# Kernel tuning notes

Measured on AMD Instinct MI355X. Metric: run time of the kernel, lower is better.

Reference implementation:

```python
import jax, jax.numpy as jnp
import numpy as np
from jax.scipy.special import digamma

N, D, K = 32768, 64, 64


def setup_inputs() -> dict:
    key = jax.random.key(0)
    k1, k2, k3, k4, k5, k6, k7 = jax.random.split(key, 7)
    X = jax.random.normal(k1, (N, D), dtype=jnp.float32)
    means = jax.random.normal(k2, (K, D), dtype=jnp.float32)
    # Upper-triangular precision Cholesky factors with strictly positive diagonal
    # (matches solve_triangular(L, I).T from the torch code).
    off = jnp.triu(jax.random.normal(k3, (K, D, D), dtype=jnp.float32) * 0.05, 1)
    diag = jnp.exp(jax.random.normal(k4, (K, D), dtype=jnp.float32) * 0.1)
    precisions_chol = off + jax.vmap(jnp.diag)(diag)
    weight_concentration = jax.random.uniform(k5, (2, K), dtype=jnp.float32, minval=0.5, maxval=5.0)
    # degrees_of_freedom must be > D - 1 so digamma args stay positive
    degrees_of_freedom = jnp.float32(D) + jax.random.uniform(k6, (K,), dtype=jnp.float32, minval=1.0, maxval=50.0)
    mean_precision = jax.random.uniform(k7, (K,), dtype=jnp.float32, minval=0.5, maxval=10.0)
    return {"X": X, "means": means, "precisions_chol": precisions_chol,
            "weight_concentration": weight_concentration,
            "degrees_of_freedom": degrees_of_freedom, "mean_precision": mean_precision}


def _weighted_log_prob(X, means, precisions_chol, weight_concentration,
                       degrees_of_freedom, mean_precision):
    n_features = X.shape[1]
    # log|prec_chol_k| = sum of log of diagonal entries
    log_det = jnp.sum(jnp.log(jnp.diagonal(precisions_chol, axis1=1, axis2=2)), axis=1)  # [K]
    # whitened residuals: y[n,k,:] = X[n] @ P_k - mu_k @ P_k
    XP = jnp.einsum('nd,kde->nke', X, precisions_chol)            # [N,K,D]
    muP = jnp.einsum('kd,kde->ke', means, precisions_chol)        # [K,D]
    sq = jnp.sum(jnp.square(XP - muP[None]), axis=-1)             # [N,K]
    log2pi = jnp.log(jnp.float32(2.0 * np.pi))
    log_gauss = -0.5 * (n_features * log2pi + sq) + log_det[None]
    # Bayesian corrections
    log_gauss = log_gauss - 0.5 * n_features * jnp.log(degrees_of_freedom)[None]
    i = jnp.arange(n_features, dtype=jnp.float32)
    log_lambda = n_features * jnp.log(jnp.float32(2.0)) + jnp.sum(
        digamma(0.5 * (degrees_of_freedom[None, :] - i[:, None])), axis=0)  # [K]
    log_prob = log_gauss + 0.5 * (log_lambda - n_features / mean_precision)[None]
    # stick-breaking log weights (dirichlet_process)
    a, b = weight_concentration[0], weight_concentration[1]
    dsum = digamma(a + b)
    log_w = digamma(a) - dsum + jnp.concatenate(
        [jnp.zeros((1,), dtype=X.dtype), jnp.cumsum(digamma(b) - dsum)[:-1]])
    return log_prob + log_w[None]


def reference(X, means, precisions_chol, weight_concentration,
              degrees_of_freedom, mean_precision):
    wlp = _weighted_log_prob(X, means, precisions_chol, weight_concentration,
                             degrees_of_freedom, mean_precision)
    return jnp.argmax(wlp, axis=1)
```

## Files before the change

### kernel.cpp

```cpp
#include <hip/hip_runtime.h>
#include <math.h>

#define N_ROWS 32768
#define DIM 64
#define KCOMP 64
#define KSPLIT 8
#define KLOCAL 8
#define THREADS 256
#define ROWS_PER_BLOCK 128
#define ROWS_PER_WAVE 32
#define ROWGROUPS (N_ROWS / ROWS_PER_BLOCK)

#define PT_K_BYTES 16384

#define LOG2PI_D 1.8378770664093454836

typedef _Float16 f16x8 __attribute__((ext_vector_type(8)));
typedef float f32x4 __attribute__((ext_vector_type(4)));

__device__ __forceinline__ double digamma_d(double x) {
  double r = 0.0;
  while (x < 6.0) { r -= 1.0 / x; x += 1.0; }
  double inv = 1.0 / x;
  double inv2 = inv * inv;
  double s = log(x) - 0.5 * inv
      - inv2 * (1.0/12.0 - inv2 * (1.0/120.0 - inv2 * (1.0/252.0
      - inv2 * (1.0/240.0 - inv2 * (1.0/132.0)))));
  return r + s;
}

__global__ void prep1_kernel(const float* __restrict__ means,
                             const float* __restrict__ P,
                             const float* __restrict__ wc,
                             const float* __restrict__ dof,
                             const float* __restrict__ mp,
                             char*   __restrict__ Pt,
                             float*  __restrict__ muP,
                             double* __restrict__ t_arr,
                             double* __restrict__ g_arr,
                             double* __restrict__ pc_arr)
{
  __shared__ float lds[DIM][DIM + 1];
  const int k = blockIdx.x;
  const int t = threadIdx.x;
  const float* Pk = P + k * DIM * DIM;

  for (int i = t; i < DIM * DIM; i += THREADS)
    lds[i >> 6][i & 63] = Pk[i];
  __syncthreads();

  char* dst = Pt + (size_t)k * PT_K_BYTES;
#pragma unroll
  for (int cc = 0; cc < 4; ++cc) {
    int cid  = cc * THREADS + t;
    int blk  = cid >> 7;
    int sel  = (cid >> 6) & 1;
    int lane = cid & 63;
    int et = blk >> 1, c = blk & 1;
    int m = lane & 15, q = lane >> 4;
    int e = et * 16 + m;
    int d0 = c * 32 + q * 8;
    f16x8 o;
#pragma unroll
    for (int j = 0; j < 8; ++j) {
      float v = lds[d0 + j][e];
      _Float16 h = (_Float16)v;
      o[j] = sel ? (_Float16)(v - (float)h) : h;
    }
    *(f16x8*)(dst + cid * 16) = o;
  }

  if (t < 64) {
    const int i = t;
    const float* mk = means + k * DIM;
    float acc = 0.f;
#pragma unroll 8
    for (int d = 0; d < DIM; ++d) acc = fmaf(mk[d], lds[d][i], acc);
    muP[k * DIM + i] = acc;

    double dofk = (double)dof[k];
    double s1 = digamma_d(0.5 * (dofk - (double)i));
    double s2 = log((double)lds[i][i]);
#pragma unroll
    for (int off = 32; off > 0; off >>= 1) {
      s1 += __shfl_down(s1, off);
      s2 += __shfl_down(s2, off);
    }
    if (i == 0) {
      double ak = (double)wc[k], bk = (double)wc[KCOMP + k];
      double dgab = digamma_d(ak + bk);
      double log_lambda = (double)DIM * log(2.0) + s1;
      double pc = s2
                - 0.5 * (double)DIM * LOG2PI_D
                - 0.5 * (double)DIM * log(dofk)
                + 0.5 * (log_lambda - (double)DIM / (double)mp[k]);
      t_arr[k] = digamma_d(bk) - dgab;
      g_arr[k] = digamma_d(ak) - dgab;
      pc_arr[k] = pc;
    }
  }
}

__global__ __launch_bounds__(THREADS, 4) void main_kernel(
    const float* __restrict__ X,
    const char*  __restrict__ Pt,
    const float* __restrict__ muP,
    const double* __restrict__ t_arr,
    const double* __restrict__ g_arr,
    const double* __restrict__ pc_arr,
    unsigned long long* __restrict__ packed,
    int* __restrict__ cnt,
    int* __restrict__ out)
{
  __shared__ float cvec_lds[KCOMP];
  __shared__ float mup_lds[KLOCAL * DIM];
  __shared__ int is_last;

  const int tid  = threadIdx.x;
  const int wave = tid >> 6;
  const int lane = tid & 63;
  const int m    = lane & 15;
  const int q    = lane >> 4;
  const int ks   = blockIdx.y;
  const int rowbase = blockIdx.x * ROWS_PER_BLOCK + wave * ROWS_PER_WAVE;

  if (tid < 64) {
    double t = t_arr[tid];
    double s = t;
#pragma unroll
    for (int off = 1; off < 64; off <<= 1) {
      double v = __shfl_up(s, off);
      if (tid >= off) s += v;
    }
    cvec_lds[tid] = (float)(pc_arr[tid] + g_arr[tid] + (s - t));
  }
  for (int i = tid; i < KLOCAL * DIM; i += THREADS)
    mup_lds[i] = muP[ks * KLOCAL * DIM + i];

  f16x8 ahi[2][2], alo[2][2];
#pragma unroll
  for (int rt = 0; rt < 2; ++rt) {
    int row = rowbase + rt * 16 + m;
    const float* xp = X + row * DIM;
#pragma unroll
    for (int c = 0; c < 2; ++c) {
      const float4* xq4 = (const float4*)(xp + c * 32 + q * 8);
      float4 v0 = xq4[0], v1 = xq4[1];
      float xv[8] = {v0.x, v0.y, v0.z, v0.w, v1.x, v1.y, v1.z, v1.w};
      f16x8 h, l;
#pragma unroll
      for (int j = 0; j < 8; ++j) {
        _Float16 hv = (_Float16)xv[j];
        h[j] = hv;
        l[j] = (_Float16)(xv[j] - (float)hv);
      }
      ahi[rt][c] = h;
      alo[rt][c] = l;
    }
  }

  __syncthreads();

  float best = -INFINITY;
  int   bidx = 0;
  const bool b0 = (m & 1), b1 = (m & 2), b2 = (m & 4);

  f16x8 pbh[2], pbl[2];
  {
    const char* pk0 = Pt + (size_t)(ks * KLOCAL) * PT_K_BYTES;
#pragma unroll
    for (int c = 0; c < 2; ++c) {
      const char* bp = pk0 + (c << 11) + (lane << 4);
      pbh[c] = *(const f16x8*)bp;
      pbl[c] = *(const f16x8*)(bp + 1024);
    }
  }

  for (int ki = 0; ki < KLOCAL; ++ki) {
    const int k = ks * KLOCAL + ki;
    const char* pk = Pt + (size_t)k * PT_K_BYTES;
    const float ck = cvec_lds[k];
    float sq[8] = {0.f,0.f,0.f,0.f,0.f,0.f,0.f,0.f};

#pragma unroll
    for (int et = 0; et < 4; ++et) {
      const float mval = -mup_lds[(ki << 6) + et * 16 + m];
      f32x4 acc[2];
#pragma unroll
      for (int rt = 0; rt < 2; ++rt)
#pragma unroll
        for (int r = 0; r < 4; ++r) acc[rt][r] = mval;

#pragma unroll
      for (int c = 0; c < 2; ++c) {
        f16x8 bh, bl;
        if (et == 0) { bh = pbh[c]; bl = pbl[c]; }
        else {
          const char* bp = pk + ((et * 2 + c) << 11) + (lane << 4);
          bh = *(const f16x8*)bp;
          bl = *(const f16x8*)(bp + 1024);
        }
#pragma unroll
        for (int rt = 0; rt < 2; ++rt) {
          acc[rt] = __builtin_amdgcn_mfma_f32_16x16x32_f16(ahi[rt][c], bh, acc[rt], 0, 0, 0);
          acc[rt] = __builtin_amdgcn_mfma_f32_16x16x32_f16(ahi[rt][c], bl, acc[rt], 0, 0, 0);
          acc[rt] = __builtin_amdgcn_mfma_f32_16x16x32_f16(alo[rt][c], bh, acc[rt], 0, 0, 0);
        }
      }
#pragma unroll
      for (int rt = 0; rt < 2; ++rt)
#pragma unroll
        for (int r = 0; r < 4; ++r)
          sq[rt * 4 + r] = fmaf(acc[rt][r], acc[rt][r], sq[rt * 4 + r]);
    }

    {
      const int kn = (ki + 1 < KLOCAL) ? (k + 1) : k;
      const char* npk = Pt + (size_t)kn * PT_K_BYTES;
#pragma unroll
      for (int c = 0; c < 2; ++c) {
        const char* bp = npk + (c << 11) + (lane << 4);
        pbh[c] = *(const f16x8*)bp;
        pbl[c] = *(const f16x8*)(bp + 1024);
      }
    }

    float w4[4];
#pragma unroll
    for (int p = 0; p < 4; ++p) {
      float keep = b0 ? sq[2*p+1] : sq[2*p];
      float send = b0 ? sq[2*p]   : sq[2*p+1];
      w4[p] = keep + __shfl_xor(send, 1);
    }
    float u2[2];
#pragma unroll
    for (int p = 0; p < 2; ++p) {
      float keep = b1 ? w4[2*p+1] : w4[2*p];
      float send = b1 ? w4[2*p]   : w4[2*p+1];
      u2[p] = keep + __shfl_xor(send, 2);
    }
    float keep = b2 ? u2[1] : u2[0];
    float send = b2 ? u2[0] : u2[1];
    float z = keep + __shfl_xor(send, 4);
    z += __shfl_xor(z, 8);

    float wv = fmaf(-0.5f, z, ck);
    if (wv > best || (wv == best && k < bidx)) { best = wv; bidx = k; }
  }

  if (m < 8) {
    int rt = (m >> 2) & 1, r = m & 3;
    int row = rowbase + rt * 16 + q * 4 + r;
    unsigned int b = __float_as_uint(best);
    unsigned int u = (b & 0x80000000u) ? ~b : (b | 0x80000000u);
    unsigned long long pkd = ((unsigned long long)u << 32)
                           | (unsigned long long)(63 - bidx);
    atomicMax(&packed[row], pkd);
  }
  __builtin_amdgcn_s_waitcnt(0);
  __syncthreads();
  if (tid == 0) {
    int old = atomicAdd(&cnt[blockIdx.x], 1);
    is_last = (old == KSPLIT - 1);
  }
  __syncthreads();
  if (is_last && tid < ROWS_PER_BLOCK) {
    int n = blockIdx.x * ROWS_PER_BLOCK + tid;
    unsigned long long p = __hip_atomic_load(&packed[n], __ATOMIC_RELAXED,
                                             __HIP_MEMORY_SCOPE_AGENT);
    out[n] = 63 - (int)(p & 63ull);
  }
}

extern "C" void kernel_launch(void* const* d_in, const int* in_sizes, int n_in,
                              void* d_out, int out_size, void* d_ws, size_t ws_size,
                              hipStream_t stream) {
  const float* X     = (const float*)d_in[0];
  const float* means = (const float*)d_in[1];
  const float* P     = (const float*)d_in[2];
  const float* wc    = (const float*)d_in[3];
  const float* dof   = (const float*)d_in[4];
  const float* mp    = (const float*)d_in[5];
  int* out = (int*)d_out;

  char* wsb = (char*)d_ws;
  float*  muP    = (float*)(wsb);
  double* t_arr  = (double*)(wsb + 16640);
  double* g_arr  = (double*)(wsb + 17152);
  double* pc_arr = (double*)(wsb + 17664);
  int*    cnt    = (int*)(wsb + 20480);
  unsigned long long* packed = (unsigned long long*)(wsb + 24576);
  char*   Pt     = wsb + 294912;

  hipMemsetAsync(wsb + 20480, 0, 286720 - 20480, stream);

  prep1_kernel<<<KCOMP, THREADS, 0, stream>>>(means, P, wc, dof, mp, Pt,
                                              muP, t_arr, g_arr, pc_arr);

  dim3 grid(ROWGROUPS, KSPLIT);
  main_kernel<<<grid, THREADS, 0, stream>>>(X, Pt, muP, t_arr, g_arr, pc_arr,
                                            packed, cnt, out);
}
```

Before: 120.9 us.

## Stage per-component precision factors in double-buffered LDS via async global-to-LDS copies

```diff
diff --git a/kernel.cpp b/kernel.cpp
--- a/kernel.cpp
+++ b/kernel.cpp
@@ -17,6 +17,14 @@
 
 typedef _Float16 f16x8 __attribute__((ext_vector_type(8)));
 typedef float f32x4 __attribute__((ext_vector_type(4)));
+
+#define AS1 __attribute__((address_space(1)))
+#define AS3 __attribute__((address_space(3)))
+
+__device__ __forceinline__ void async_copy16(const char* g, char* l) {
+  __builtin_amdgcn_global_load_lds((const AS1 unsigned int*)g,
+                                   (AS3 unsigned int*)l, 16, 0, 0);
+}
 
 __device__ __forceinline__ double digamma_d(double x) {
   double r = 0.0;
@@ -112,6 +120,7 @@
     int* __restrict__ cnt,
     int* __restrict__ out)
 {
+  __shared__ uint4 bbuf[2][PT_K_BYTES / 16];
   __shared__ float cvec_lds[KCOMP];
   __shared__ float mup_lds[KLOCAL * DIM];
   __shared__ int is_last;
@@ -123,6 +132,17 @@
   const int q    = lane >> 4;
   const int ks   = blockIdx.y;
   const int rowbase = blockIdx.x * ROWS_PER_BLOCK + wave * ROWS_PER_WAVE;
+  const int k0   = ks * KLOCAL;
+
+  {
+    const char* src = Pt + (size_t)k0 * PT_K_BYTES;
+#pragma unroll
+    for (int i = 0; i < 4; ++i) {
+      const int g = wave * 4 + i;
+      async_copy16(src + (g << 10) + (lane << 4),
+                   (char*)&bbuf[0][g << 6]);
+    }
+  }
 
   if (tid < 64) {
     double t = t_arr[tid];
@@ -165,20 +185,21 @@
   int   bidx = 0;
   const bool b0 = (m & 1), b1 = (m & 2), b2 = (m & 4);
 
-  f16x8 pbh[2], pbl[2];
-  {
-    const char* pk0 = Pt + (size_t)(ks * KLOCAL) * PT_K_BYTES;
-#pragma unroll
-    for (int c = 0; c < 2; ++c) {
-      const char* bp = pk0 + (c << 11) + (lane << 4);
-      pbh[c] = *(const f16x8*)bp;
-      pbl[c] = *(const f16x8*)(bp + 1024);
-    }
-  }
-
   for (int ki = 0; ki < KLOCAL; ++ki) {
-    const int k = ks * KLOCAL + ki;
-    const char* pk = Pt + (size_t)k * PT_K_BYTES;
+    const int k = k0 + ki;
+    const int p = ki & 1;
+
+    if (ki + 1 < KLOCAL) {
+      const char* src = Pt + (size_t)(k + 1) * PT_K_BYTES;
+#pragma unroll
+      for (int i = 0; i < 4; ++i) {
+        const int g = wave * 4 + i;
+        async_copy16(src + (g << 10) + (lane << 4),
+                     (char*)&bbuf[1 - p][g << 6]);
+      }
+    }
+
+    const char* lb = (const char*)bbuf[p];
     const float ck = cvec_lds[k];
     float sq[8] = {0.f,0.f,0.f,0.f,0.f,0.f,0.f,0.f};
 
@@ -193,13 +214,9 @@
 
 #pragma unroll
       for (int c = 0; c < 2; ++c) {
-        f16x8 bh, bl;
-        if (et == 0) { bh = pbh[c]; bl = pbl[c]; }
-        else {
-          const char* bp = pk + ((et * 2 + c) << 11) + (lane << 4);
-          bh = *(const f16x8*)bp;
-          bl = *(const f16x8*)(bp + 1024);
-        }
+        const char* bp = lb + ((et * 2 + c) << 11) + (lane << 4);
+        f16x8 bh = *(const f16x8*)bp;
+        f16x8 bl = *(const f16x8*)(bp + 1024);
 #pragma unroll
         for (int rt = 0; rt < 2; ++rt) {
           acc[rt] = __builtin_amdgcn_mfma_f32_16x16x32_f16(ahi[rt][c], bh, acc[rt], 0, 0, 0);
@@ -214,30 +231,19 @@
           sq[rt * 4 + r] = fmaf(acc[rt][r], acc[rt][r], sq[rt * 4 + r]);
     }
 
-    {
-      const int kn = (ki + 1 < KLOCAL) ? (k + 1) : k;
-      const char* npk = Pt + (size_t)kn * PT_K_BYTES;
-#pragma unroll
-      for (int c = 0; c < 2; ++c) {
-        const char* bp = npk + (c << 11) + (lane << 4);
-        pbh[c] = *(const f16x8*)bp;
-        pbl[c] = *(const f16x8*)(bp + 1024);
-      }
-    }
-
     float w4[4];
 #pragma unroll
-    for (int p = 0; p < 4; ++p) {
-      float keep = b0 ? sq[2*p+1] : sq[2*p];
-      float send = b0 ? sq[2*p]   : sq[2*p+1];
-      w4[p] = keep + __shfl_xor(send, 1);
+    for (int pp = 0; pp < 4; ++pp) {
+      float keep = b0 ? sq[2*pp+1] : sq[2*pp];
+      float send = b0 ? sq[2*pp]   : sq[2*pp+1];
+      w4[pp] = keep + __shfl_xor(send, 1);
     }
     float u2[2];
 #pragma unroll
-    for (int p = 0; p < 2; ++p) {
-      float keep = b1 ? w4[2*p+1] : w4[2*p];
-      float send = b1 ? w4[2*p]   : w4[2*p+1];
-      u2[p] = keep + __shfl_xor(send, 2);
+    for (int pp = 0; pp < 2; ++pp) {
+      float keep = b1 ? w4[2*pp+1] : w4[2*pp];
+      float send = b1 ? w4[2*pp]   : w4[2*pp+1];
+      u2[pp] = keep + __shfl_xor(send, 2);
     }
     float keep = b2 ? u2[1] : u2[0];
     float send = b2 ? u2[0] : u2[1];
@@ -246,6 +252,8 @@
 
     float wv = fmaf(-0.5f, z, ck);
     if (wv > best || (wv == best && k < bidx)) { best = wv; bidx = k; }
+
+    __syncthreads();
   }
 
   if (m < 8) {
@@ -266,9 +274,9 @@
   __syncthreads();
   if (is_last && tid < ROWS_PER_BLOCK) {
     int n = blockIdx.x * ROWS_PER_BLOCK + tid;
-    unsigned long long p = __hip_atomic_load(&packed[n], __ATOMIC_RELAXED,
-                                             __HIP_MEMORY_SCOPE_AGENT);
-    out[n] = 63 - (int)(p & 63ull);
+    unsigned long long pv = __hip_atomic_load(&packed[n], __ATOMIC_RELAXED,
+                                              __HIP_MEMORY_SCOPE_AGENT);
+    out[n] = 63 - (int)(pv & 63ull);
   }
 }
 
```

New measurement: 118.5 us. 1.02x faster.
